# Kernel optimization log

Hardware: AMD Instinct MI355X
Metric: run time of the kernel (lower is better)

The kernel has to match this reference:

```python
import jax, jax.numpy as jnp
import numpy as np

THRESHOLD = 1.0   # spiking threshold (also used for reset detection)
BETA = 0.95       # reservoir membrane decay
N = 2048          # reservoir_size


def _heaviside(x):
    # snntorch Heaviside: (x > 0).float()
    return (x > 0).astype(x.dtype)


def setup_inputs() -> dict:
    key = jax.random.key(0)
    k1, k2, k3 = jax.random.split(key, 3)
    B, T = 32, 500
    x = jax.random.normal(k1, (B, T, 1), dtype=jnp.float32)
    # recurrent connectivity matrix loaded from .npy in the original; random here
    W = jax.random.normal(k2, (N, N), dtype=jnp.float32) / jnp.sqrt(jnp.float32(N))
    # nn.Linear default bias init: U(-1/sqrt(N), 1/sqrt(N))
    bound = 1.0 / np.sqrt(N)
    b = jax.random.uniform(k3, (N,), dtype=jnp.float32, minval=-bound, maxval=bound)
    return {"x": x, "W": W, "b": b}


def reference(x, W, b):
    """RLeaky reservoir with reset_mechanism='zero', reset_delay=True.
    Per step (snntorch RLeaky semantics):
      reset   = heaviside(mem_prev - threshold)            (detached)
      base    = beta*mem_prev + input + W @ spk_prev + b
      mem_new = base - reset*base                          ('zero' reset)
      spk_new = heaviside(mem_new - threshold)
    Input current = scalar x_t broadcast across all N neurons.
    """
    B = x.shape[0]
    Wt = W.T  # (N, N), spk @ W.T == Linear(spk)

    def step(carry, x_t):
        spk, mem = carry  # each (B, N)
        reset = _heaviside(mem - THRESHOLD)
        base = BETA * mem + x_t + spk @ Wt + b  # x_t: (B,1) broadcasts over N
        mem_new = base * (1.0 - reset)
        spk_new = _heaviside(mem_new - THRESHOLD)
        return (spk_new, mem_new), (spk_new, mem_new)

    init = (jnp.zeros((B, N), x.dtype), jnp.zeros((B, N), x.dtype))
    xs = jnp.swapaxes(x, 0, 1)  # (T, B, 1)
    _, (spk_rec, mem_rec) = jax.lax.scan(step, init, xs)
    avg_firing_rate = spk_rec.mean()
    return avg_firing_rate, spk_rec, mem_rec
```

## Files before the change

### kernel.cpp

```cpp
#include <hip/hip_runtime.h>

#define NN 2048
#define NB 32
#define NT 500
#define WGS 512
#define NWG 256


__global__ void init_kernel(unsigned int* __restrict__ bitsG, int* __restrict__ spkcnt) {
    int g = blockIdx.x * blockDim.x + threadIdx.x;
    if (g < NN) bitsG[g] = 0u;
    if (g == 0) *spkcnt = 0;
}

__launch_bounds__(WGS)
__global__ void step_kernel(const float* __restrict__ x,
                            const float* __restrict__ W,
                            const float* __restrict__ bias,
                            float* __restrict__ out,
                            unsigned int* __restrict__ bitsG,
                            int* __restrict__ spkcnt,
                            int step)
{
    __shared__ unsigned int lbits[NN];
    __shared__ float lpart[8][8][32];
    __shared__ float lout[2][NB][9];
    __shared__ int   lcnt[4];

    const int wg = blockIdx.x;
    const int t  = threadIdx.x;
    const int i0 = wg * 8;
    const int cur = step & 1;

    ((uint4*)lbits)[t] = ((const uint4*)(bitsG + (size_t)cur * NN))[t];

    const int rh4 = (t >> 8) * 4;
    const int jh  = (t >> 5) & 7;
    const int b   = t & 31;

    const float4* __restrict__ wr0 = (const float4*)(W + (size_t)(i0 + rh4 + 0) * NN) + jh * 64;
    const float4* __restrict__ wr1 = (const float4*)(W + (size_t)(i0 + rh4 + 1) * NN) + jh * 64;
    const float4* __restrict__ wr2 = (const float4*)(W + (size_t)(i0 + rh4 + 2) * NN) + jh * 64;
    const float4* __restrict__ wr3 = (const float4*)(W + (size_t)(i0 + rh4 + 3) * NN) + jh * 64;

    __syncthreads();

    float c0 = 0.0f, c1 = 0.0f, c2 = 0.0f, c3 = 0.0f;
    const uint4* bp = ((const uint4*)lbits) + jh * 64;
    #pragma unroll 2
    for (int jj = 0; jj < 64; ++jj) {
        const float4 w0 = wr0[jj];
        const float4 w1 = wr1[jj];
        const float4 w2 = wr2[jj];
        const float4 w3 = wr3[jj];
        const uint4  bu = bp[jj];
        float s;
        s = (float)((bu.x >> b) & 1u);
        c0 = fmaf(w0.x, s, c0); c1 = fmaf(w1.x, s, c1);
        c2 = fmaf(w2.x, s, c2); c3 = fmaf(w3.x, s, c3);
        s = (float)((bu.y >> b) & 1u);
        c0 = fmaf(w0.y, s, c0); c1 = fmaf(w1.y, s, c1);
        c2 = fmaf(w2.y, s, c2); c3 = fmaf(w3.y, s, c3);
        s = (float)((bu.z >> b) & 1u);
        c0 = fmaf(w0.z, s, c0); c1 = fmaf(w1.z, s, c1);
        c2 = fmaf(w2.z, s, c2); c3 = fmaf(w3.z, s, c3);
        s = (float)((bu.w >> b) & 1u);
        c0 = fmaf(w0.w, s, c0); c1 = fmaf(w1.w, s, c1);
        c2 = fmaf(w2.w, s, c2); c3 = fmaf(w3.w, s, c3);
    }
    lpart[jh][rh4 + 0][b] = c0;
    lpart[jh][rh4 + 1][b] = c1;
    lpart[jh][rh4 + 2][b] = c2;
    lpart[jh][rh4 + 3][b] = c3;
    __syncthreads();

    if (t < 256) {
        const int cil = t >> 5;
        const int cb  = t & 31;

        float d = lpart[0][cil][cb];
        #pragma unroll
        for (int k = 1; k < 8; ++k) d += lpart[k][cil][cb];

        float mem = 0.0f, sp = 0.0f;
        if (step > 0) {
            size_t po = ((size_t)(step - 1) * NB + cb) * (size_t)NN + i0 + cil;
            mem = out[1 + (size_t)NT * NB * NN + po];
            sp  = out[1 + po];
        }

        float xv   = x[(size_t)cb * NT + step];
        float base = 0.95f * mem + xv + d + bias[i0 + cil];
        float nm   = base * (1.0f - sp);
        float ns   = (nm > 1.0f) ? 1.0f : 0.0f;

        unsigned long long bal = __ballot(ns > 0.5f);
        unsigned int* bw = bitsG + (size_t)(1 - cur) * NN;
        const int l  = t & 63;
        const int w2 = t >> 6;
        if (l == 0)  bw[i0 + 2 * w2]     = (unsigned int)(bal & 0xFFFFFFFFull);
        if (l == 32) bw[i0 + 2 * w2 + 1] = (unsigned int)(bal >> 32);
        if (l == 0)  lcnt[w2] = __popcll(bal);

        lout[0][cb][cil] = ns;
        lout[1][cb][cil] = nm;
    }
    __syncthreads();

    if (t == 0) {
        int s = lcnt[0] + lcnt[1] + lcnt[2] + lcnt[3];
        if (s) atomicAdd(spkcnt, s);
    }

    {
        float* spk_rec = out + 1;
        float* mem_rec = out + 1 + (size_t)NT * NB * NN;
        const int arr = t >> 8;
        const int r2  = t & 255;
        const int bb  = r2 >> 3;
        const int il  = r2 & 7;
        size_t o = ((size_t)step * NB + bb) * (size_t)NN + i0 + il;
        if (arr == 0) spk_rec[o] = lout[0][bb][il];
        else          mem_rec[o] = lout[1][bb][il];
    }
}

__global__ void final_kernel(float* __restrict__ out, const int* __restrict__ spkcnt) {
    out[0] = (float)((double)(*spkcnt) / (double)((long long)NT * NB * NN));
}

extern "C" void kernel_launch(void* const* d_in, const int* in_sizes, int n_in,
                              void* d_out, int out_size, void* d_ws, size_t ws_size,
                              hipStream_t stream) {
    const float* x    = (const float*)d_in[0];
    const float* W    = (const float*)d_in[1];
    const float* bias = (const float*)d_in[2];
    float* out = (float*)d_out;

    unsigned int* bitsG  = (unsigned int*)d_ws;
    int*          spkcnt = (int*)((char*)d_ws + 2 * NN * 4);

    init_kernel<<<dim3(8), dim3(256), 0, stream>>>(bitsG, spkcnt);
    for (int step = 0; step < NT; ++step) {
        step_kernel<<<dim3(NWG), dim3(WGS), 0, stream>>>(x, W, bias, out,
                                                         bitsG, spkcnt, step);
    }
    final_kernel<<<dim3(1), dim3(1), 0, stream>>>(out, spkcnt);
}
```

Measured before the change: 9.977 ms.

## Double workgroup size, keep membrane state in compact workspace, drop global atomic

Each workgroup now runs 1024 threads with 2 weight rows per thread instead of 4, which raises the thread count working on the per-step matvec. The previous membrane value is read from a compact neuron-major workspace and the previous spike from the shared bit vector, instead of strided reads from the large output arrays. Inputs are transposed once for coalesced access, the global atomic spike counter becomes per-workgroup counters summed in the final kernel, and output stores are nontemporal. The larger block raises register and occupancy pressure, and it adds a workspace write each step.

Result: faster. 9.404 ms (-5.7%).

```diff
diff --git a/kernel.cpp b/kernel.cpp
--- a/kernel.cpp
+++ b/kernel.cpp
@@ -3,23 +3,30 @@
 #define NN 2048
 #define NB 32
 #define NT 500
-#define WGS 512
+#define WGS 1024
 #define NWG 256
 
 
-__global__ void init_kernel(unsigned int* __restrict__ bitsG, int* __restrict__ spkcnt) {
+__global__ void init_kernel(const float* __restrict__ x,
+                            unsigned int* __restrict__ bitsG,
+                            float* __restrict__ mem_ws,
+                            float* __restrict__ xT,
+                            int* __restrict__ wgcnt) {
     int g = blockIdx.x * blockDim.x + threadIdx.x;
-    if (g < NN) bitsG[g] = 0u;
-    if (g == 0) *spkcnt = 0;
+    if (g < 2 * NN) bitsG[g] = 0u;
+    if (g < NN * NB) mem_ws[g] = 0.0f;
+    if (g < NT * NB) xT[g] = x[(size_t)(g & 31) * NT + (g >> 5)];
+    if (g < NWG) wgcnt[g] = 0;
 }
 
-__launch_bounds__(WGS)
-__global__ void step_kernel(const float* __restrict__ x,
-                            const float* __restrict__ W,
+__launch_bounds__(WGS, 4)
+__global__ void step_kernel(const float* __restrict__ W,
                             const float* __restrict__ bias,
                             float* __restrict__ out,
                             unsigned int* __restrict__ bitsG,
-                            int* __restrict__ spkcnt,
+                            float* __restrict__ mem_ws,
+                            const float* __restrict__ xT,
+                            int* __restrict__ wgcnt,
                             int step)
 {
     __shared__ unsigned int lbits[NN];
@@ -32,46 +39,40 @@
     const int i0 = wg * 8;
     const int cur = step & 1;
 
-    ((uint4*)lbits)[t] = ((const uint4*)(bitsG + (size_t)cur * NN))[t];
+    ((uint2*)lbits)[t] = ((const uint2*)(bitsG + (size_t)cur * NN))[t];
 
-    const int rh4 = (t >> 8) * 4;
-    const int jh  = (t >> 5) & 7;
-    const int b   = t & 31;
+    const int rh = t >> 8;
+    const int jh = (t >> 5) & 7;
+    const int b  = t & 31;
 
-    const float4* __restrict__ wr0 = (const float4*)(W + (size_t)(i0 + rh4 + 0) * NN) + jh * 64;
-    const float4* __restrict__ wr1 = (const float4*)(W + (size_t)(i0 + rh4 + 1) * NN) + jh * 64;
-    const float4* __restrict__ wr2 = (const float4*)(W + (size_t)(i0 + rh4 + 2) * NN) + jh * 64;
-    const float4* __restrict__ wr3 = (const float4*)(W + (size_t)(i0 + rh4 + 3) * NN) + jh * 64;
+    float mem = 0.0f, xv = 0.0f, biasv = 0.0f;
+    if (t < 256) {
+        const int cil = t >> 5, cb = t & 31;
+        mem   = mem_ws[(size_t)(i0 + cil) * NB + cb];
+        xv    = xT[step * NB + cb];
+        biasv = bias[i0 + cil];
+    }
+
+    const float4* __restrict__ wr0 = (const float4*)(W + (size_t)(i0 + 2 * rh    ) * NN) + jh * 64;
+    const float4* __restrict__ wr1 = (const float4*)(W + (size_t)(i0 + 2 * rh + 1) * NN) + jh * 64;
 
     __syncthreads();
 
-    float c0 = 0.0f, c1 = 0.0f, c2 = 0.0f, c3 = 0.0f;
+    float c0 = 0.0f, c1 = 0.0f;
     const uint4* bp = ((const uint4*)lbits) + jh * 64;
-    #pragma unroll 2
+    #pragma unroll 4
     for (int jj = 0; jj < 64; ++jj) {
         const float4 w0 = wr0[jj];
         const float4 w1 = wr1[jj];
-        const float4 w2 = wr2[jj];
-        const float4 w3 = wr3[jj];
         const uint4  bu = bp[jj];
         float s;
-        s = (float)((bu.x >> b) & 1u);
-        c0 = fmaf(w0.x, s, c0); c1 = fmaf(w1.x, s, c1);
-        c2 = fmaf(w2.x, s, c2); c3 = fmaf(w3.x, s, c3);
-        s = (float)((bu.y >> b) & 1u);
-        c0 = fmaf(w0.y, s, c0); c1 = fmaf(w1.y, s, c1);
-        c2 = fmaf(w2.y, s, c2); c3 = fmaf(w3.y, s, c3);
-        s = (float)((bu.z >> b) & 1u);
-        c0 = fmaf(w0.z, s, c0); c1 = fmaf(w1.z, s, c1);
-        c2 = fmaf(w2.z, s, c2); c3 = fmaf(w3.z, s, c3);
-        s = (float)((bu.w >> b) & 1u);
-        c0 = fmaf(w0.w, s, c0); c1 = fmaf(w1.w, s, c1);
-        c2 = fmaf(w2.w, s, c2); c3 = fmaf(w3.w, s, c3);
+        s = (float)((bu.x >> b) & 1u); c0 = fmaf(w0.x, s, c0); c1 = fmaf(w1.x, s, c1);
+        s = (float)((bu.y >> b) & 1u); c0 = fmaf(w0.y, s, c0); c1 = fmaf(w1.y, s, c1);
+        s = (float)((bu.z >> b) & 1u); c0 = fmaf(w0.z, s, c0); c1 = fmaf(w1.z, s, c1);
+        s = (float)((bu.w >> b) & 1u); c0 = fmaf(w0.w, s, c0); c1 = fmaf(w1.w, s, c1);
     }
-    lpart[jh][rh4 + 0][b] = c0;
-    lpart[jh][rh4 + 1][b] = c1;
-    lpart[jh][rh4 + 2][b] = c2;
-    lpart[jh][rh4 + 3][b] = c3;
+    lpart[jh][2 * rh    ][b] = c0;
+    lpart[jh][2 * rh + 1][b] = c1;
     __syncthreads();
 
     if (t < 256) {
@@ -82,17 +83,13 @@
         #pragma unroll
         for (int k = 1; k < 8; ++k) d += lpart[k][cil][cb];
 
-        float mem = 0.0f, sp = 0.0f;
-        if (step > 0) {
-            size_t po = ((size_t)(step - 1) * NB + cb) * (size_t)NN + i0 + cil;
-            mem = out[1 + (size_t)NT * NB * NN + po];
-            sp  = out[1 + po];
-        }
+        float sp = (float)((lbits[i0 + cil] >> cb) & 1u);
 
-        float xv   = x[(size_t)cb * NT + step];
-        float base = 0.95f * mem + xv + d + bias[i0 + cil];
+        float base = 0.95f * mem + xv + d + biasv;
         float nm   = base * (1.0f - sp);
         float ns   = (nm > 1.0f) ? 1.0f : 0.0f;
+
+        mem_ws[(size_t)(i0 + cil) * NB + cb] = nm;
 
         unsigned long long bal = __ballot(ns > 0.5f);
         unsigned int* bw = bitsG + (size_t)(1 - cur) * NN;
@@ -107,12 +104,9 @@
     }
     __syncthreads();
 
-    if (t == 0) {
-        int s = lcnt[0] + lcnt[1] + lcnt[2] + lcnt[3];
-        if (s) atomicAdd(spkcnt, s);
-    }
+    if (t == 0) wgcnt[wg] += lcnt[0] + lcnt[1] + lcnt[2] + lcnt[3];
 
-    {
+    if (t < 512) {
         float* spk_rec = out + 1;
         float* mem_rec = out + 1 + (size_t)NT * NB * NN;
         const int arr = t >> 8;
@@ -120,13 +114,15 @@
         const int bb  = r2 >> 3;
         const int il  = r2 & 7;
         size_t o = ((size_t)step * NB + bb) * (size_t)NN + i0 + il;
-        if (arr == 0) spk_rec[o] = lout[0][bb][il];
-        else          mem_rec[o] = lout[1][bb][il];
+        if (arr == 0) __builtin_nontemporal_store(lout[0][bb][il], &spk_rec[o]);
+        else          __builtin_nontemporal_store(lout[1][bb][il], &mem_rec[o]);
     }
 }
 
-__global__ void final_kernel(float* __restrict__ out, const int* __restrict__ spkcnt) {
-    out[0] = (float)((double)(*spkcnt) / (double)((long long)NT * NB * NN));
+__global__ void final_kernel(float* __restrict__ out, const int* __restrict__ wgcnt) {
+    long long s = 0;
+    for (int k = 0; k < NWG; ++k) s += wgcnt[k];
+    out[0] = (float)((double)s / (double)((long long)NT * NB * NN));
 }
 
 extern "C" void kernel_launch(void* const* d_in, const int* in_sizes, int n_in,
@@ -138,12 +134,14 @@
     float* out = (float*)d_out;
 
     unsigned int* bitsG  = (unsigned int*)d_ws;
-    int*          spkcnt = (int*)((char*)d_ws + 2 * NN * 4);
+    float*        mem_ws = (float*)((char*)d_ws + 16384);
+    float*        xT     = (float*)((char*)d_ws + 278528);
+    int*          wgcnt  = (int*)((char*)d_ws + 344064);
 
-    init_kernel<<<dim3(8), dim3(256), 0, stream>>>(bitsG, spkcnt);
+    init_kernel<<<dim3(256), dim3(256), 0, stream>>>(x, bitsG, mem_ws, xT, wgcnt);
     for (int step = 0; step < NT; ++step) {
-        step_kernel<<<dim3(NWG), dim3(WGS), 0, stream>>>(x, W, bias, out,
-                                                         bitsG, spkcnt, step);
+        step_kernel<<<dim3(NWG), dim3(WGS), 0, stream>>>(W, bias, out, bitsG,
+                                                         mem_ws, xT, wgcnt, step);
     }
-    final_kernel<<<dim3(1), dim3(1), 0, stream>>>(out, spkcnt);
+    final_kernel<<<dim3(1), dim3(1), 0, stream>>>(out, wgcnt);
 }
```
